# Kernel optimization log

Hardware: AMD Instinct MI355X
Metric: run time of the kernel (lower is better)

## Reference

```python
import jax, jax.numpy as jnp
import numpy as np

N = 262144      # total nodes
D = 256         # feature channels
B = 1024        # number of graphs (fixed segment count)
EPS = 1e-05


def setup_inputs() -> dict:
    key = jax.random.key(0)
    k1, k2 = jax.random.split(key)
    x = jax.random.normal(k1, (N, D), dtype=jnp.float32)
    batch = jnp.sort(jax.random.randint(k2, (N,), 0, B, dtype=jnp.int64))
    weight = jnp.ones((D,), dtype=jnp.float32)
    bias = jnp.zeros((D,), dtype=jnp.float32)
    return {"x": x, "batch": batch, "weight": weight, "bias": bias}


def reference(x, batch, weight, bias):
    # degree per graph, clamped to >=1, times D (per-graph element count)
    deg = jax.ops.segment_sum(jnp.ones((x.shape[0],), dtype=x.dtype), batch, num_segments=B)
    norm = jnp.clip(deg, 1.0, None)[:, None] * x.shape[-1]          # [B,1]
    # per-graph scalar mean over all nodes and channels
    mean = jax.ops.segment_sum(x, batch, num_segments=B).sum(-1, keepdims=True) / norm  # [B,1]
    xc = x - mean[batch]                                             # [N,D]
    var = jax.ops.segment_sum(xc * xc, batch, num_segments=B).sum(-1, keepdims=True) / norm  # [B,1]
    out = xc / (jnp.sqrt(var)[batch] + EPS)                          # note: eps added after sqrt, as in source
    return out * weight + bias
```

## Files before the change

kernel.cpp:

```cpp
#include <hip/hip_runtime.h>

#define NN 262144
#define DD 256
#define BB 1024
#define GEPS 1e-5f
#define NCHUNK 16

__global__ __launch_bounds__(1024) void k_main(const float4* __restrict__ x,
                                               const int* __restrict__ batch,
                                               const float4* __restrict__ w,
                                               const float4* __restrict__ bi,
                                               float4* __restrict__ out) {
    __shared__ int   s_coarse[2];
    __shared__ int   s_pos[2];
    __shared__ float red_s[16];
    __shared__ float red_q[16];
    __shared__ float bc[2];

    const int b    = blockIdx.x;
    const int tid  = threadIdx.x;
    const int wid  = tid >> 6;
    const int lane = tid & 63;

    if (tid < 2) s_coarse[tid] = NN;
    __syncthreads();
    {
        const int idx = tid << 8;
        const int v   = batch[idx];
        if (v >= b)     atomicMin(&s_coarse[0], idx);
        if (v >= b + 1) atomicMin(&s_coarse[1], idx);
    }
    __syncthreads();
    {
        const int k = tid >> 8;
        const int t = tid & 255;
        if (k < 2) {
            const int tgt = b + k;
            const int cc  = s_coarse[k];
            const int i   = cc - 255 + t;
            if (i >= 0) {
                const int vi  = (i < NN) ? batch[i] : 0x7fffffff;
                const int vim = (i > 0) ? batch[i - 1] : (-2147483647 - 1);
                if (vi >= tgt && vim < tgt) s_pos[k] = i;
            }
        }
    }
    __syncthreads();
    const int s0 = s_pos[0];
    const int s1 = s_pos[1];
    if (s1 <= s0) return;

    float s = 0.0f, q = 0.0f;
    float4 v[NCHUNK];
    const int rbase = s0 + wid;
    #pragma unroll
    for (int i = 0; i < NCHUNK; ++i) {
        const int r = rbase + i * 16;
        if (r < s1) {
            float4 t4 = x[r * 64 + lane];
            s += t4.x + t4.y + t4.z + t4.w;
            q += t4.x * t4.x + t4.y * t4.y + t4.z * t4.z + t4.w * t4.w;
            asm volatile("" : "+v"(t4.x), "+v"(t4.y), "+v"(t4.z), "+v"(t4.w));
            v[i] = t4;
        }
    }
    for (int r = rbase + NCHUNK * 16; r < s1; r += 16) {
        const float4 t4 = x[r * 64 + lane];
        s += t4.x + t4.y + t4.z + t4.w;
        q += t4.x * t4.x + t4.y * t4.y + t4.z * t4.z + t4.w * t4.w;
    }

    #pragma unroll
    for (int off = 32; off; off >>= 1) {
        s += __shfl_down(s, off, 64);
        q += __shfl_down(q, off, 64);
    }
    if (lane == 0) { red_s[wid] = s; red_q[wid] = q; }
    __syncthreads();
    if (tid == 0) {
        float ts = 0.0f, tq = 0.0f;
        #pragma unroll
        for (int i = 0; i < 16; ++i) { ts += red_s[i]; tq += red_q[i]; }
        const float norm = (float)(s1 - s0) * (float)DD;
        const float mean = ts / norm;
        const float var  = fmaxf(tq / norm - mean * mean, 0.0f);
        bc[0] = mean;
        bc[1] = 1.0f / (sqrtf(var) + GEPS);
    }
    __syncthreads();
    const float  mean = bc[0];
    const float  inv  = bc[1];
    const float4 wv   = w[lane];
    const float4 bv   = bi[lane];

    #pragma unroll
    for (int i = 0; i < NCHUNK; ++i) {
        const int r = rbase + i * 16;
        if (r < s1) {
            float4 o;
            o.x = (v[i].x - mean) * inv * wv.x + bv.x;
            o.y = (v[i].y - mean) * inv * wv.y + bv.y;
            o.z = (v[i].z - mean) * inv * wv.z + bv.z;
            o.w = (v[i].w - mean) * inv * wv.w + bv.w;
            out[r * 64 + lane] = o;
        }
    }
    for (int r = rbase + NCHUNK * 16; r < s1; r += 16) {
        const float4 t4 = x[r * 64 + lane];
        float4 o;
        o.x = (t4.x - mean) * inv * wv.x + bv.x;
        o.y = (t4.y - mean) * inv * wv.y + bv.y;
        o.z = (t4.z - mean) * inv * wv.z + bv.z;
        o.w = (t4.w - mean) * inv * wv.w + bv.w;
        out[r * 64 + lane] = o;
    }
}

extern "C" void kernel_launch(void* const* d_in, const int* in_sizes, int n_in,
                              void* d_out, int out_size, void* d_ws, size_t ws_size,
                              hipStream_t stream) {
    const float4* x     = (const float4*)d_in[0];
    const int*    batch = (const int*)d_in[1];
    const float4* w     = (const float4*)d_in[2];
    const float4* bi    = (const float4*)d_in[3];
    float4*       out   = (float4*)d_out;

    k_main<<<BB, 1024, 0, stream>>>(x, batch, w, bi, out);
}
```

Baseline: 131.9 us.

## Process four graphs per block, overlapping next-graph loads with current-graph stores

Each block now handles four consecutive graphs and launches a quarter as many blocks. Inside the block, loading and reducing the next graph is interleaved with normalizing and storing the current one, so memory reads and writes overlap. Output stores become nontemporal, and the coarse boundary search is generalized to five boundaries per block. The cost is fewer blocks (256 on a large GPU), which lowers parallelism and occupancy, plus extra syncthreads between graphs.

```diff
diff --git a/kernel.cpp b/kernel.cpp
--- a/kernel.cpp
+++ b/kernel.cpp
@@ -4,59 +4,69 @@
 #define DD 256
 #define BB 1024
 #define GEPS 1e-5f
+#define GPB 4
+#define NBLK (BB / GPB)
 #define NCHUNK 16
+
+typedef float floatx4 __attribute__((ext_vector_type(4)));
 
 __global__ __launch_bounds__(1024) void k_main(const float4* __restrict__ x,
                                                const int* __restrict__ batch,
                                                const float4* __restrict__ w,
                                                const float4* __restrict__ bi,
                                                float4* __restrict__ out) {
-    __shared__ int   s_coarse[2];
-    __shared__ int   s_pos[2];
+    __shared__ int   s_coarse[GPB + 1];
+    __shared__ int   s_bound[GPB + 1];
     __shared__ float red_s[16];
     __shared__ float red_q[16];
     __shared__ float bc[2];
 
-    const int b    = blockIdx.x;
+    const int g0   = blockIdx.x * GPB;
     const int tid  = threadIdx.x;
     const int wid  = tid >> 6;
     const int lane = tid & 63;
 
-    if (tid < 2) s_coarse[tid] = NN;
+    if (tid <= GPB) s_coarse[tid] = NN;
     __syncthreads();
     {
         const int idx = tid << 8;
         const int v   = batch[idx];
-        if (v >= b)     atomicMin(&s_coarse[0], idx);
-        if (v >= b + 1) atomicMin(&s_coarse[1], idx);
+        const int pv  = __shfl_up(v, 1, 64);
+        #pragma unroll
+        for (int k = 0; k <= GPB; ++k) {
+            const int tgt = g0 + k;
+            if (v >= tgt && (lane == 0 || pv < tgt))
+                atomicMin(&s_coarse[k], idx);
+        }
     }
     __syncthreads();
     {
-        const int k = tid >> 8;
-        const int t = tid & 255;
-        if (k < 2) {
-            const int tgt = b + k;
+        const int sub = tid >> 8;
+        const int t   = tid & 255;
+        for (int k = sub; k <= GPB; k += 4) {
+            const int tgt = g0 + k;
             const int cc  = s_coarse[k];
             const int i   = cc - 255 + t;
             if (i >= 0) {
                 const int vi  = (i < NN) ? batch[i] : 0x7fffffff;
                 const int vim = (i > 0) ? batch[i - 1] : (-2147483647 - 1);
-                if (vi >= tgt && vim < tgt) s_pos[k] = i;
+                if (vi >= tgt && vim < tgt) s_bound[k] = i;
             }
         }
     }
     __syncthreads();
-    const int s0 = s_pos[0];
-    const int s1 = s_pos[1];
-    if (s1 <= s0) return;
 
-    float s = 0.0f, q = 0.0f;
+    const float4 wv = w[lane];
+    const float4 bv = bi[lane];
+
     float4 v[NCHUNK];
-    const int rbase = s0 + wid;
+    float  s = 0.0f, q = 0.0f;
+    int sA = s_bound[0], eA = s_bound[1];
+
     #pragma unroll
     for (int i = 0; i < NCHUNK; ++i) {
-        const int r = rbase + i * 16;
-        if (r < s1) {
+        const int r = sA + wid + i * 16;
+        if (r < eA) {
             float4 t4 = x[r * 64 + lane];
             s += t4.x + t4.y + t4.z + t4.w;
             q += t4.x * t4.x + t4.y * t4.y + t4.z * t4.z + t4.w * t4.w;
@@ -64,55 +74,81 @@
             v[i] = t4;
         }
     }
-    for (int r = rbase + NCHUNK * 16; r < s1; r += 16) {
+    for (int r = sA + wid + NCHUNK * 16; r < eA; r += 16) {
         const float4 t4 = x[r * 64 + lane];
         s += t4.x + t4.y + t4.z + t4.w;
         q += t4.x * t4.x + t4.y * t4.y + t4.z * t4.z + t4.w * t4.w;
     }
 
     #pragma unroll
-    for (int off = 32; off; off >>= 1) {
-        s += __shfl_down(s, off, 64);
-        q += __shfl_down(q, off, 64);
-    }
-    if (lane == 0) { red_s[wid] = s; red_q[wid] = q; }
-    __syncthreads();
-    if (tid == 0) {
-        float ts = 0.0f, tq = 0.0f;
+    for (int g = 0; g < GPB; ++g) {
+        float rs = s, rq = q;
         #pragma unroll
-        for (int i = 0; i < 16; ++i) { ts += red_s[i]; tq += red_q[i]; }
-        const float norm = (float)(s1 - s0) * (float)DD;
-        const float mean = ts / norm;
-        const float var  = fmaxf(tq / norm - mean * mean, 0.0f);
-        bc[0] = mean;
-        bc[1] = 1.0f / (sqrtf(var) + GEPS);
-    }
-    __syncthreads();
-    const float  mean = bc[0];
-    const float  inv  = bc[1];
-    const float4 wv   = w[lane];
-    const float4 bv   = bi[lane];
+        for (int off = 32; off; off >>= 1) {
+            rs += __shfl_down(rs, off, 64);
+            rq += __shfl_down(rq, off, 64);
+        }
+        if (lane == 0) { red_s[wid] = rs; red_q[wid] = rq; }
+        __syncthreads();
+        if (tid == 0) {
+            float ts = 0.0f, tq = 0.0f;
+            #pragma unroll
+            for (int i = 0; i < 16; ++i) { ts += red_s[i]; tq += red_q[i]; }
+            const float norm = fmaxf((float)(eA - sA), 1.0f) * (float)DD;
+            const float mean = ts / norm;
+            const float var  = fmaxf(tq / norm - mean * mean, 0.0f);
+            bc[0] = mean;
+            bc[1] = 1.0f / (sqrtf(var) + GEPS);
+        }
+        __syncthreads();
+        const float mean = bc[0];
+        const float inv  = bc[1];
+        __syncthreads();
 
-    #pragma unroll
-    for (int i = 0; i < NCHUNK; ++i) {
-        const int r = rbase + i * 16;
-        if (r < s1) {
-            float4 o;
-            o.x = (v[i].x - mean) * inv * wv.x + bv.x;
-            o.y = (v[i].y - mean) * inv * wv.y + bv.y;
-            o.z = (v[i].z - mean) * inv * wv.z + bv.z;
-            o.w = (v[i].w - mean) * inv * wv.w + bv.w;
-            out[r * 64 + lane] = o;
+        const bool haveNext = (g + 1 < GPB);
+        const int  sB = haveNext ? s_bound[g + 1] : 0;
+        const int  eB = haveNext ? s_bound[g + 2] : 0;
+        s = 0.0f; q = 0.0f;
+
+        #pragma unroll
+        for (int i = 0; i < NCHUNK; ++i) {
+            const int ro = sA + wid + i * 16;
+            if (ro < eA) {
+                floatx4 o;
+                o.x = (v[i].x - mean) * inv * wv.x + bv.x;
+                o.y = (v[i].y - mean) * inv * wv.y + bv.y;
+                o.z = (v[i].z - mean) * inv * wv.z + bv.z;
+                o.w = (v[i].w - mean) * inv * wv.w + bv.w;
+                __builtin_nontemporal_store(o, (floatx4*)&out[ro * 64 + lane]);
+            }
+            if (haveNext) {
+                const int ri = sB + wid + i * 16;
+                if (ri < eB) {
+                    float4 t4 = x[ri * 64 + lane];
+                    s += t4.x + t4.y + t4.z + t4.w;
+                    q += t4.x * t4.x + t4.y * t4.y + t4.z * t4.z + t4.w * t4.w;
+                    asm volatile("" : "+v"(t4.x), "+v"(t4.y), "+v"(t4.z), "+v"(t4.w));
+                    v[i] = t4;
+                }
+            }
         }
-    }
-    for (int r = rbase + NCHUNK * 16; r < s1; r += 16) {
-        const float4 t4 = x[r * 64 + lane];
-        float4 o;
-        o.x = (t4.x - mean) * inv * wv.x + bv.x;
-        o.y = (t4.y - mean) * inv * wv.y + bv.y;
-        o.z = (t4.z - mean) * inv * wv.z + bv.z;
-        o.w = (t4.w - mean) * inv * wv.w + bv.w;
-        out[r * 64 + lane] = o;
+        for (int r = sA + wid + NCHUNK * 16; r < eA; r += 16) {
+            const float4 t4 = x[r * 64 + lane];
+            floatx4 o;
+            o.x = (t4.x - mean) * inv * wv.x + bv.x;
+            o.y = (t4.y - mean) * inv * wv.y + bv.y;
+            o.z = (t4.z - mean) * inv * wv.z + bv.z;
+            o.w = (t4.w - mean) * inv * wv.w + bv.w;
+            __builtin_nontemporal_store(o, (floatx4*)&out[r * 64 + lane]);
+        }
+        if (haveNext) {
+            for (int r = sB + wid + NCHUNK * 16; r < eB; r += 16) {
+                const float4 t4 = x[r * 64 + lane];
+                s += t4.x + t4.y + t4.z + t4.w;
+                q += t4.x * t4.x + t4.y * t4.y + t4.z * t4.z + t4.w * t4.w;
+            }
+        }
+        sA = sB; eA = eB;
     }
 }
 
@@ -125,5 +161,5 @@
     const float4* bi    = (const float4*)d_in[3];
     float4*       out   = (float4*)d_out;
 
-    k_main<<<BB, 1024, 0, stream>>>(x, batch, w, bi, out);
+    k_main<<<NBLK, 1024, 0, stream>>>(x, batch, w, bi, out);
 }
```

After: 149.5 us. 13.3% more time.
